# Optimization experiments

Measured on AMD Instinct MI355X. Metric: run time of the kernel, lower is better.

## Reference

```python
import jax, jax.numpy as jnp
import numpy as np

# ---- static config (mirrors Spectral2xDown.__init__) ----
B, C_IN, C_OUT = 2, 256, 256
H_HI, W_HI = 256, 512
H_LO, W_LO = 128, 256
LMAX = H_LO            # 128
MMAX = W_LO // 2 + 1   # 129
GROUPS = 32
EPS_GN = 1e-5


def _cc_nodes_weights(n):
    """Clenshaw-Curtis nodes x_j=cos(pi*j/(n-1)) and quadrature weights on [-1,1]
    (torch_harmonics 'equiangular' grid)."""
    N = n - 1
    tj = np.pi * np.arange(n) / N
    xj = np.cos(tj)
    ks = np.arange(1, N // 2 + 1)
    b = np.where(2 * ks == N, 1.0, 2.0)
    s = (b / (4.0 * ks**2 - 1.0))[None, :] * np.cos(2.0 * ks[None, :] * tj[:, None])
    w = (2.0 / N) * (1.0 - s.sum(axis=1))
    w[0] = w[-1] = (1.0 / N**2) if (N % 2) else (1.0 / (N**2 - 1.0))
    return xj, w


def _legpoly(mmax, lmax, x):
    """Orthonormal associated Legendre (-1)^m c_lm P_lm(x), shape [mmax,lmax,len(x)]
    (torch_harmonics _precompute_legpoly, norm='ortho', csphase=True)."""
    nmax = max(mmax, lmax)
    vdm = np.zeros((nmax, nmax, len(x)))
    vdm[0, 0] = 1.0 / np.sqrt(4.0 * np.pi)
    for l in range(1, nmax):
        vdm[l - 1, l] = np.sqrt(2 * l + 1) * x * vdm[l - 1, l - 1]
        vdm[l, l] = np.sqrt((2 * l + 1) * (1 + x) * (1 - x) / (2 * l)) * vdm[l - 1, l - 1]
    for l in range(2, nmax):
        for m in range(0, l - 1):
            vdm[m, l] = (x * np.sqrt((2 * l - 1) / (l - m) * (2 * l + 1) / (l + m)) * vdm[m, l - 1]
                         - np.sqrt((l + m - 1) / (l - m) * (2 * l + 1) / (2 * l - 3)
                                   * (l - m - 1) / (l + m)) * vdm[m, l - 2])
    vdm = vdm[:mmax, :lmax].copy()
    for m in range(1, mmax, 2):  # Condon-Shortley phase
        vdm[m] *= -1.0
    return vdm


def _precompute():
    ct_hi, w_hi = _cc_nodes_weights(H_HI)
    pct_hi = _legpoly(MMAX, LMAX, np.flip(np.arccos(ct_hi)) * 0 + np.cos(np.flip(np.arccos(ct_hi))))
    wmat_hi = pct_hi * w_hi[None, None, :]          # quadrature folded in: [M,L,K_hi]
    ct_lo, _ = _cc_nodes_weights(H_LO)
    pct_lo = _legpoly(MMAX, LMAX, np.cos(np.flip(np.arccos(ct_lo))))  # [M,L,K_lo]
    return wmat_hi.astype(np.float32), pct_lo.astype(np.float32)


def setup_inputs() -> dict:
    key = jax.random.key(0)
    k1, k2 = jax.random.split(key, 2)
    x = jax.random.normal(k1, (B, C_IN, H_HI, W_HI), jnp.float32)
    conv_w = jax.random.normal(k2, (C_OUT, C_IN), jnp.float32) / np.sqrt(C_IN)
    conv_b = jnp.zeros((C_OUT,), jnp.float32)
    gamma = jnp.ones((C_OUT,), jnp.float32)
    beta = jnp.zeros((C_OUT,), jnp.float32)
    wmat_hi, pct_lo = _precompute()
    return {"x": x, "conv_w": conv_w, "conv_b": conv_b, "gamma": gamma, "beta": beta,
            "wmat_hi": jnp.asarray(wmat_hi), "pct_lo": jnp.asarray(pct_lo)}


def reference(x, conv_w, conv_b, gamma, beta, wmat_hi, pct_lo):
    # --- forward real SHT on high-res grid (2*pi * rfft(norm='forward') + Legendre quadrature) ---
    X = (2.0 * jnp.pi / W_HI) * jnp.fft.rfft(x, axis=-1)     # [B,C,K_hi,W_HI//2+1]
    X = X[..., :MMAX]                                        # truncate to mmax
    flm_r = jnp.einsum('bckm,mlk->bclm', X.real, wmat_hi)    # [B,C,L,M]
    flm_i = jnp.einsum('bckm,mlk->bclm', X.imag, wmat_hi)
    # --- inverse real SHT on low-res grid ---
    g = (jnp.einsum('bclm,mlk->bckm', flm_r, pct_lo)
         + 1j * jnp.einsum('bclm,mlk->bckm', flm_i, pct_lo))  # [B,C,K_lo,M]
    y = jnp.fft.irfft(g, n=W_LO, axis=-1) * W_LO             # irfft norm='forward'
    # --- 1x1 conv -> GroupNorm(32) -> exact GELU ---
    h = jnp.einsum('bchw,oc->bohw', y, conv_w) + conv_b[None, :, None, None]
    hg = h.reshape(B, GROUPS, C_OUT // GROUPS, H_LO, W_LO)
    mu = hg.mean(axis=(2, 3, 4), keepdims=True)
    var = ((hg - mu) ** 2).mean(axis=(2, 3, 4), keepdims=True)
    hn = ((hg - mu) * jax.lax.rsqrt(var + EPS_GN)).reshape(B, C_OUT, H_LO, W_LO)
    out = hn * gamma[None, :, None, None] + beta[None, :, None, None]
    return jax.nn.gelu(out, approximate=False)
```

## Files before the change

### kernel.cpp

```cpp
#include <hip/hip_runtime.h>
#include <math.h>


#define ROWS_HI 131072
#define ROWS_LO 65536

#define B_FT    0LL
#define B_FIT   262144LL
#define B_WM    393216LL
#define B_PCT   8781824LL
#define B_WB    12976128LL
#define B_STATS 13107200LL
#define B_R1    13107712LL
#define B_R2    80216576LL

typedef __attribute__((ext_vector_type(8))) short bf16x8;
typedef __attribute__((ext_vector_type(8))) unsigned short ushort8;
typedef __attribute__((ext_vector_type(4))) unsigned short ushort4v;
typedef __attribute__((ext_vector_type(4))) float f32x4;

__device__ inline unsigned short f2bf(float f){
  unsigned int u = __float_as_uint(f);
  unsigned int r = u + 0x7FFFu + ((u >> 16) & 1u);
  return (unsigned short)(r >> 16);
}

__global__ __launch_bounds__(256) void k_tables(unsigned char* __restrict__ ws){
  unsigned short* FT  = (unsigned short*)(ws + B_FT);
  unsigned short* FIT = (unsigned short*)(ws + B_FIT);
  float* stats = (float*)(ws + B_STATS);
  int idx = blockIdx.x*256 + threadIdx.x;
  if (idx < 131072){
    int p = idx >> 9, w = idx & 511, m = p >> 1;
    int pr = (m*w) & 511;
    float ang = (float)pr * (float)(2.0*M_PI/512.0);
    float s, c; sincosf(ang, &s, &c);
    const float S = (float)(2.0*M_PI/512.0);
    FT[idx] = f2bf((p & 1) ? (-S*s) : (S*c));
  }
  int i2 = idx - 131072;
  if (i2 >= 0 && i2 < 65536){
    int w = i2 >> 8, p = i2 & 255, m = p >> 1;
    float eps = (m == 0) ? 1.f : 2.f;
    int pr = (m*w) & 255;
    float ang = (float)pr * (float)(2.0*M_PI/256.0);
    float s, c; sincosf(ang, &s, &c);
    FIT[i2] = f2bf((p & 1) ? (-eps*s) : (eps*c));
  }
  int i3 = idx - (131072 + 65536);
  if (i3 >= 0 && i3 < 128) stats[i3] = 0.f;
}

__global__ __launch_bounds__(256) void k_prep(const float* __restrict__ wmat,
                                              const float* __restrict__ pct,
                                              const float* __restrict__ Wc,
                                              unsigned char* __restrict__ ws){
  unsigned short* WM = (unsigned short*)(ws + B_WM);
  unsigned short* PT = (unsigned short*)(ws + B_PCT);
  unsigned short* WB = (unsigned short*)(ws + B_WB);
  int idx = blockIdx.x*256 + threadIdx.x;
  if (idx < 4194304){
    WM[idx] = f2bf(wmat[idx]);
  } else if (idx < 6291456){
    int j = idx - 4194304;
    int m = j >> 14, kp = (j >> 7) & 127, l = j & 127;
    PT[j] = f2bf(pct[m*16384 + l*128 + kp]);
  } else if (idx < 6356992){
    int j = idx - 6291456;
    WB[j] = f2bf(Wc[j]);
  }
}

template<int AMODE, int CMODE, bool BIAS, int MT, int NT, int SKIP>
__global__ __launch_bounds__(256) void k_gemm(
    const float* __restrict__ Af,
    const unsigned short* __restrict__ Abf,
    const unsigned short* __restrict__ Bt,
    float* __restrict__ Cf,
    unsigned short* __restrict__ Cbf,
    const float* __restrict__ bias,
    int ldA, int ldB, int ldC, int ksteps,
    long long sA, long long sB, int bzsh, long long sC)
{
  constexpr int BM = MT*32;
  constexpr int BN = NT*32;
  __shared__ unsigned short As[BM][40];
  __shared__ unsigned short Bs[BN][40];
  const int tid = threadIdx.x;
  const int z = blockIdx.z;
  const int m = z >> 1;
  const long long offA = (long long)z * sA;
  const long long offB = (long long)(z >> bzsh) * sB;
  const long long offC = (long long)z * sC;
  const int row0 = blockIdx.x * BM;
  const int n0   = blockIdx.y * BN;
  const int lane = tid & 63;
  const int wv = tid >> 6;
  const int wm = wv >> 1, wn = wv & 1;
  const int fr = lane & 15, q = lane >> 4;

  f32x4 acc[MT][NT];
#pragma unroll
  for (int i=0;i<MT;++i)
#pragma unroll
    for (int j=0;j<NT;++j) acc[i][j] = (f32x4){0.f,0.f,0.f,0.f};

  int ks0 = (SKIP == 2) ? (m >> 5) : 0;
  for (int ks = ks0; ks < ksteps; ++ks){
    const int k0 = ks * 32;
    if (AMODE == 0){
      const int row = tid >> 1, half = tid & 1;
      const float* s = Af + offA + (long long)(row0 + row) * ldA + k0 + half*16;
      float vv[16];
      *(float4*)(vv+0)  = *(const float4*)(s+0);
      *(float4*)(vv+4)  = *(const float4*)(s+4);
      *(float4*)(vv+8)  = *(const float4*)(s+8);
      *(float4*)(vv+12) = *(const float4*)(s+12);
      ushort8 H0, H1;
#pragma unroll
      for (int j=0;j<8;++j){ H0[j] = f2bf(vv[j]); H1[j] = f2bf(vv[8+j]); }
      *(ushort8*)&As[row][half*16]   = H0;
      *(ushort8*)&As[row][half*16+8] = H1;
    } else if (BM == 256){
      const unsigned short* s = Abf + offA + (long long)(row0 + tid) * ldA + k0;
      *(ushort8*)&As[tid][0]  = *(const ushort8*)(s);
      *(ushort8*)&As[tid][8]  = *(const ushort8*)(s+8);
      *(ushort8*)&As[tid][16] = *(const ushort8*)(s+16);
      *(ushort8*)&As[tid][24] = *(const ushort8*)(s+24);
    } else {
      const int row = tid >> 1, half = tid & 1;
      const unsigned short* s = Abf + offA + (long long)(row0 + row) * ldA + k0 + half*16;
      *(ushort8*)&As[row][half*16]   = *(const ushort8*)(s);
      *(ushort8*)&As[row][half*16+8] = *(const ushort8*)(s+8);
    }
    if (BN == 256){
      const unsigned short* s = Bt + offB + (long long)(n0 + tid) * ldB + k0;
      *(ushort8*)&Bs[tid][0]  = *(const ushort8*)(s);
      *(ushort8*)&Bs[tid][8]  = *(const ushort8*)(s+8);
      *(ushort8*)&Bs[tid][16] = *(const ushort8*)(s+16);
      *(ushort8*)&Bs[tid][24] = *(const ushort8*)(s+24);
    } else {
      const int row = tid >> 1, half = tid & 1;
      const unsigned short* s = Bt + offB + (long long)(n0 + row) * ldB + k0 + half*16;
      *(ushort8*)&Bs[row][half*16]   = *(const ushort8*)(s);
      *(ushort8*)&Bs[row][half*16+8] = *(const ushort8*)(s+8);
    }
    __syncthreads();
    bf16x8 ah[MT];
#pragma unroll
    for (int mt=0;mt<MT;++mt)
      ah[mt] = *(const bf16x8*)&As[wm*(MT*16)+mt*16+fr][q*8];
#pragma unroll
    for (int nt=0;nt<NT;++nt){
      if (SKIP == 1 && (wn*(NT*16) + nt*16 + 16 <= m)) continue;
      bf16x8 bb = *(const bf16x8*)&Bs[wn*(NT*16)+nt*16+fr][q*8];
#pragma unroll
      for (int mt=0;mt<MT;++mt)
        acc[mt][nt] = __builtin_amdgcn_mfma_f32_16x16x32_bf16(ah[mt], bb, acc[mt][nt], 0,0,0);
    }
    __syncthreads();
  }

  if (CMODE == 0){
#pragma unroll
    for (int mt=0;mt<MT;++mt){
      int row = row0 + wm*(MT*16) + mt*16 + q*4;
      float bv0=0.f,bv1=0.f,bv2=0.f,bv3=0.f;
      if (BIAS){ bv0=bias[row]; bv1=bias[row+1]; bv2=bias[row+2]; bv3=bias[row+3]; }
#pragma unroll
      for (int nt=0;nt<NT;++nt){
        int col = n0 + wn*(NT*16) + nt*16 + fr;
        float* dst = Cf + offC + (long long)row * ldC + col;
        dst[0]                = acc[mt][nt][0] + bv0;
        dst[(long long)ldC]   = acc[mt][nt][1] + bv1;
        dst[(long long)ldC*2] = acc[mt][nt][2] + bv2;
        dst[(long long)ldC*3] = acc[mt][nt][3] + bv3;
      }
    }
  } else if (CMODE == 1){
#pragma unroll
    for (int nt=0;nt<NT;++nt){
      int colp = n0 + wn*(NT*16) + nt*16 + fr;
#pragma unroll
      for (int mt=0;mt<MT;++mt){
        int rowb = row0 + wm*(MT*16) + mt*16 + q*4;
        ushort4v h;
        h[0] = f2bf(acc[mt][nt][0]);
        h[1] = f2bf(acc[mt][nt][1]);
        h[2] = f2bf(acc[mt][nt][2]);
        h[3] = f2bf(acc[mt][nt][3]);
        *(ushort4v*)&Cbf[offC + (long long)colp * ldC + rowb] = h;
      }
    }
  } else {
#pragma unroll
    for (int mt=0;mt<MT;++mt){
      int row = row0 + wm*(MT*16) + mt*16 + q*4;
#pragma unroll
      for (int nt=0;nt<NT;++nt){
        int col = n0 + wn*(NT*16) + nt*16 + fr;
        unsigned short* dst = Cbf + offC + (long long)row * ldC + col;
        dst[0]      = f2bf(acc[mt][nt][0]);
        dst[ldC]    = f2bf(acc[mt][nt][1]);
        dst[ldC*2]  = f2bf(acc[mt][nt][2]);
        dst[ldC*3]  = f2bf(acc[mt][nt][3]);
      }
    }
  }
}

__global__ __launch_bounds__(256) void k_trb(const unsigned short* __restrict__ g,
                                             unsigned short* __restrict__ gT){
  __shared__ unsigned short t[64][68];
  const int r0 = blockIdx.x * 64;
  const int p0 = blockIdx.y * 64;
  const int tr = threadIdx.x & 15, tc = threadIdx.x >> 4;
#pragma unroll
  for (int i=0;i<4;++i){
    int pl = tc + i*16;
    ushort4v v = *(const ushort4v*)(g + (long long)(p0+pl)*ROWS_LO + r0 + tr*4);
    *(ushort4v*)&t[pl][tr*4] = v;
  }
  __syncthreads();
#pragma unroll
  for (int i=0;i<4;++i){
    int rl = tc + i*16;
    ushort4v w;
    w[0]=t[tr*4+0][rl]; w[1]=t[tr*4+1][rl]; w[2]=t[tr*4+2][rl]; w[3]=t[tr*4+3][rl];
    *(ushort4v*)(gT + (long long)(r0+rl)*256 + p0 + tr*4) = w;
  }
}

__global__ __launch_bounds__(256) void k_tr2(const float* __restrict__ y,
                                             unsigned short* __restrict__ yT){
  __shared__ float t[64][65];
  const int s0 = blockIdx.x * 64;
  const int c0 = blockIdx.y * 64;
  const int b  = blockIdx.z;
  const int tr = threadIdx.x & 15, tc = threadIdx.x >> 4;
#pragma unroll
  for (int i=0;i<4;++i){
    int cl = tc + i*16;
    float4 v = *(const float4*)(y + (long long)b*8388608 + (long long)(c0+cl)*32768 + s0 + tr*4);
    t[cl][tr*4+0]=v.x; t[cl][tr*4+1]=v.y; t[cl][tr*4+2]=v.z; t[cl][tr*4+3]=v.w;
  }
  __syncthreads();
#pragma unroll
  for (int i=0;i<4;++i){
    int sl = tc + i*16;
    ushort4v w;
    w[0]=f2bf(t[tr*4+0][sl]); w[1]=f2bf(t[tr*4+1][sl]);
    w[2]=f2bf(t[tr*4+2][sl]); w[3]=f2bf(t[tr*4+3][sl]);
    *(ushort4v*)(yT + (long long)b*8388608 + (long long)(s0+sl)*256 + c0 + tr*4) = w;
  }
}

__global__ __launch_bounds__(256) void k_stats(const float* __restrict__ h,
                                               float* __restrict__ stats){
  const int bg = blockIdx.y;
  const int j  = blockIdx.x;
  const int t  = threadIdx.x;
  const float* base = h + (long long)bg*262144 + j*8192;
  float s = 0.f, ss = 0.f;
#pragma unroll
  for (int i=0;i<8;++i){
    float4 v = *(const float4*)(base + i*1024 + t*4);
    s  += v.x + v.y + v.z + v.w;
    ss += v.x*v.x + v.y*v.y + v.z*v.z + v.w*v.w;
  }
#pragma unroll
  for (int off=32; off>0; off>>=1){
    s  += __shfl_down(s, off, 64);
    ss += __shfl_down(ss, off, 64);
  }
  __shared__ float red[8];
  int wid = t >> 6;
  if ((t & 63) == 0){ red[wid*2] = s; red[wid*2+1] = ss; }
  __syncthreads();
  if (t == 0){
    float S  = red[0]+red[2]+red[4]+red[6];
    float SS = red[1]+red[3]+red[5]+red[7];
    atomicAdd(&stats[bg*2+0], S);
    atomicAdd(&stats[bg*2+1], SS);
  }
}

__global__ __launch_bounds__(256) void k_norm(float* __restrict__ out,
                                              const float* __restrict__ stats,
                                              const float* __restrict__ gamma,
                                              const float* __restrict__ beta){
  long long idx4 = ((long long)blockIdx.x*256 + threadIdx.x)*4;
  int o = (int)((idx4 >> 15) & 255);
  int b = (int)(idx4 >> 23);
  int bg = b*32 + (o >> 3);
  const float inv_n = 1.0f/262144.0f;
  float mean = stats[bg*2+0] * inv_n;
  float var  = stats[bg*2+1] * inv_n - mean*mean;
  float sc = rsqrtf(var + 1e-5f);
  float ga = gamma[o], be = beta[o];
  float4 v = *(float4*)(out + idx4);
  float t0 = (v.x - mean)*sc*ga + be;
  float t1 = (v.y - mean)*sc*ga + be;
  float t2 = (v.z - mean)*sc*ga + be;
  float t3 = (v.w - mean)*sc*ga + be;
  const float ISQ2 = 0.70710678118654752f;
  v.x = 0.5f*t0*(1.0f + erff(t0*ISQ2));
  v.y = 0.5f*t1*(1.0f + erff(t1*ISQ2));
  v.z = 0.5f*t2*(1.0f + erff(t2*ISQ2));
  v.w = 0.5f*t3*(1.0f + erff(t3*ISQ2));
  *(float4*)(out + idx4) = v;
}

extern "C" void kernel_launch(void* const* d_in, const int* in_sizes, int n_in,
                              void* d_out, int out_size, void* d_ws, size_t ws_size,
                              hipStream_t stream){
  const float* x      = (const float*)d_in[0];
  const float* conv_w = (const float*)d_in[1];
  const float* conv_b = (const float*)d_in[2];
  const float* gamma  = (const float*)d_in[3];
  const float* beta   = (const float*)d_in[4];
  const float* wmat   = (const float*)d_in[5];
  const float* pct    = (const float*)d_in[6];
  unsigned char* ws = (unsigned char*)d_ws;

  unsigned short* FT   = (unsigned short*)(ws + B_FT);
  unsigned short* FIT  = (unsigned short*)(ws + B_FIT);
  unsigned short* WM   = (unsigned short*)(ws + B_WM);
  unsigned short* PT   = (unsigned short*)(ws + B_PCT);
  unsigned short* WB   = (unsigned short*)(ws + B_WB);
  float*          stats= (float*)(ws + B_STATS);
  unsigned short* Xbf  = (unsigned short*)(ws + B_R1);
  unsigned short* gb   = (unsigned short*)(ws + B_R1);
  float*          y    = (float*)(ws + B_R1);
  unsigned short* flmb = (unsigned short*)(ws + B_R2);
  unsigned short* gTb  = (unsigned short*)(ws + B_R2);
  unsigned short* yT   = (unsigned short*)(ws + B_R2);
  float* out = (float*)d_out;

  k_tables<<<769, 256, 0, stream>>>(ws);
  k_prep  <<<24832, 256, 0, stream>>>(wmat, pct, conv_w, ws);

  k_gemm<0,1,false,4,8,0><<<dim3(1024,1,1), 256, 0, stream>>>(
      x, nullptr, FT, nullptr, Xbf, nullptr, 512, 512, ROWS_HI, 16, 0, 0, 0, 0);
  k_gemm<1,2,false,4,4,1><<<dim3(4,1,256), 256, 0, stream>>>(
      nullptr, Xbf, WM, nullptr, flmb, nullptr, 256, 256, 128, 8,
      131072LL, 32768LL, 1, 65536LL);
  k_gemm<1,2,false,4,4,2><<<dim3(4,1,256), 256, 0, stream>>>(
      nullptr, flmb, PT, nullptr, gb, nullptr, 128, 128, 128, 4,
      65536LL, 16384LL, 1, 65536LL);
  k_trb<<<dim3(1024,4), 256, 0, stream>>>(gb, gTb);
  k_gemm<1,0,false,4,8,0><<<dim3(512,1,1), 256, 0, stream>>>(
      nullptr, gTb, FIT, y, nullptr, nullptr, 256, 256, 256, 8, 0, 0, 0, 0);
  k_tr2<<<dim3(512,4,2), 256, 0, stream>>>(y, yT);
  k_gemm<1,0,true,8,4,0><<<dim3(1,256,2), 256, 0, stream>>>(
      nullptr, WB, yT, out, nullptr, conv_b, 256, 256, 32768, 8,
      0, 8388608LL, 0, 8388608LL);

  k_stats<<<dim3(32,64), 256, 0, stream>>>(out, stats);
  k_norm <<<16384, 256, 0, stream>>>(out, stats, gamma, beta);
}
```

Measured before the change: 672.7 us.

## Fold forward and inverse Legendre matrices into one precomputed operator; use direct LDS loads

Multiplies the per-m inverse Legendre table by the forward quadrature matrix once per call, so the two chained per-m GEMMs become a single 256-to-128 GEMM on the Fourier coefficients. GEMM staging now uses global_load_lds 16-byte async copies into unpadded LDS tiles, with a fixed 128x128 tile and an occupancy hint. Workspace buffers stop aliasing each other. The fused operator is built in bf16, which adds rounding to the combined matrix, drops the triangular skip optimizations, and the unpadded LDS rows may cause bank conflicts.

```diff
diff --git a/kernel.cpp b/kernel.cpp
--- a/kernel.cpp
+++ b/kernel.cpp
@@ -11,8 +11,13 @@
 #define B_PCT   8781824LL
 #define B_WB    12976128LL
 #define B_STATS 13107200LL
-#define B_R1    13107712LL
-#define B_R2    80216576LL
+#define B_WMT   13107712LL
+#define B_QM    21496320LL
+#define B_XBF   29884928LL
+#define B_GB    96993792LL
+#define B_GTB   130548224LL
+#define B_Y     164102656LL
+#define B_YT    231211520LL
 
 typedef __attribute__((ext_vector_type(8))) short bf16x8;
 typedef __attribute__((ext_vector_type(8))) unsigned short ushort8;
@@ -23,6 +28,12 @@
   unsigned int u = __float_as_uint(f);
   unsigned int r = u + 0x7FFFu + ((u >> 16) & 1u);
   return (unsigned short)(r >> 16);
+}
+
+__device__ inline void gl_lds16(const unsigned short* g, unsigned short* l){
+  __builtin_amdgcn_global_load_lds(
+      (const __attribute__((address_space(1))) unsigned int*)g,
+      (__attribute__((address_space(3))) unsigned int*)l, 16, 0, 0);
 }
 
 __global__ __launch_bounds__(256) void k_tables(unsigned char* __restrict__ ws){
@@ -55,9 +66,10 @@
                                               const float* __restrict__ pct,
                                               const float* __restrict__ Wc,
                                               unsigned char* __restrict__ ws){
-  unsigned short* WM = (unsigned short*)(ws + B_WM);
-  unsigned short* PT = (unsigned short*)(ws + B_PCT);
-  unsigned short* WB = (unsigned short*)(ws + B_WB);
+  unsigned short* WM  = (unsigned short*)(ws + B_WM);
+  unsigned short* PT  = (unsigned short*)(ws + B_PCT);
+  unsigned short* WB  = (unsigned short*)(ws + B_WB);
+  unsigned short* WMT = (unsigned short*)(ws + B_WMT);
   int idx = blockIdx.x*256 + threadIdx.x;
   if (idx < 4194304){
     WM[idx] = f2bf(wmat[idx]);
@@ -68,11 +80,15 @@
   } else if (idx < 6356992){
     int j = idx - 6291456;
     WB[j] = f2bf(Wc[j]);
-  }
-}
-
-template<int AMODE, int CMODE, bool BIAS, int MT, int NT, int SKIP>
-__global__ __launch_bounds__(256) void k_gemm(
+  } else if (idx < 10551296){
+    int j = idx - 6356992;
+    int m = j >> 15, k = (j >> 7) & 255, l = j & 127;
+    WMT[j] = f2bf(wmat[m*32768 + l*256 + k]);
+  }
+}
+
+template<int AMODE, int CMODE, bool BIAS, int SKIP, int MZSH, int WPE>
+__global__ __launch_bounds__(256, WPE) void k_gemm(
     const float* __restrict__ Af,
     const unsigned short* __restrict__ Abf,
     const unsigned short* __restrict__ Bt,
@@ -82,30 +98,29 @@
     int ldA, int ldB, int ldC, int ksteps,
     long long sA, long long sB, int bzsh, long long sC)
 {
-  constexpr int BM = MT*32;
-  constexpr int BN = NT*32;
-  __shared__ unsigned short As[BM][40];
-  __shared__ unsigned short Bs[BN][40];
+  __shared__ __align__(16) unsigned short As[128][32];
+  __shared__ __align__(16) unsigned short Bs[128][32];
   const int tid = threadIdx.x;
   const int z = blockIdx.z;
-  const int m = z >> 1;
+  const int m = z >> MZSH;
   const long long offA = (long long)z * sA;
   const long long offB = (long long)(z >> bzsh) * sB;
   const long long offC = (long long)z * sC;
-  const int row0 = blockIdx.x * BM;
-  const int n0   = blockIdx.y * BN;
+  const int row0 = blockIdx.x * 128;
+  const int n0   = blockIdx.y * 128;
   const int lane = tid & 63;
   const int wv = tid >> 6;
   const int wm = wv >> 1, wn = wv & 1;
   const int fr = lane & 15, q = lane >> 4;
-
-  f32x4 acc[MT][NT];
-#pragma unroll
-  for (int i=0;i<MT;++i)
-#pragma unroll
-    for (int j=0;j<NT;++j) acc[i][j] = (f32x4){0.f,0.f,0.f,0.f};
-
-  int ks0 = (SKIP == 2) ? (m >> 5) : 0;
+  const int srow = tid >> 2, skb = tid & 3;
+
+  f32x4 acc[4][4];
+#pragma unroll
+  for (int i=0;i<4;++i)
+#pragma unroll
+    for (int j=0;j<4;++j) acc[i][j] = (f32x4){0.f,0.f,0.f,0.f};
+
+  const int ks0 = (SKIP == 2) ? (m >> 5) : 0;
   for (int ks = ks0; ks < ksteps; ++ks){
     const int k0 = ks * 32;
     if (AMODE == 0){
@@ -121,41 +136,28 @@
       for (int j=0;j<8;++j){ H0[j] = f2bf(vv[j]); H1[j] = f2bf(vv[8+j]); }
       *(ushort8*)&As[row][half*16]   = H0;
       *(ushort8*)&As[row][half*16+8] = H1;
-    } else if (BM == 256){
-      const unsigned short* s = Abf + offA + (long long)(row0 + tid) * ldA + k0;
-      *(ushort8*)&As[tid][0]  = *(const ushort8*)(s);
-      *(ushort8*)&As[tid][8]  = *(const ushort8*)(s+8);
-      *(ushort8*)&As[tid][16] = *(const ushort8*)(s+16);
-      *(ushort8*)&As[tid][24] = *(const ushort8*)(s+24);
     } else {
-      const int row = tid >> 1, half = tid & 1;
-      const unsigned short* s = Abf + offA + (long long)(row0 + row) * ldA + k0 + half*16;
-      *(ushort8*)&As[row][half*16]   = *(const ushort8*)(s);
-      *(ushort8*)&As[row][half*16+8] = *(const ushort8*)(s+8);
-    }
-    if (BN == 256){
-      const unsigned short* s = Bt + offB + (long long)(n0 + tid) * ldB + k0;
-      *(ushort8*)&Bs[tid][0]  = *(const ushort8*)(s);
-      *(ushort8*)&Bs[tid][8]  = *(const ushort8*)(s+8);
-      *(ushort8*)&Bs[tid][16] = *(const ushort8*)(s+16);
-      *(ushort8*)&Bs[tid][24] = *(const ushort8*)(s+24);
-    } else {
-      const int row = tid >> 1, half = tid & 1;
-      const unsigned short* s = Bt + offB + (long long)(n0 + row) * ldB + k0 + half*16;
-      *(ushort8*)&Bs[row][half*16]   = *(const ushort8*)(s);
-      *(ushort8*)&Bs[row][half*16+8] = *(const ushort8*)(s+8);
+#pragma unroll
+      for (int i=0;i<2;++i){
+        const unsigned short* g = Abf + offA + (long long)(row0 + i*64 + srow) * ldA + k0 + skb*8;
+        gl_lds16(g, (unsigned short*)As + i*2048 + wv*512);
+      }
+    }
+#pragma unroll
+    for (int i=0;i<2;++i){
+      const unsigned short* g = Bt + offB + (long long)(n0 + i*64 + srow) * ldB + k0 + skb*8;
+      gl_lds16(g, (unsigned short*)Bs + i*2048 + wv*512);
     }
     __syncthreads();
-    bf16x8 ah[MT];
-#pragma unroll
-    for (int mt=0;mt<MT;++mt)
-      ah[mt] = *(const bf16x8*)&As[wm*(MT*16)+mt*16+fr][q*8];
-#pragma unroll
-    for (int nt=0;nt<NT;++nt){
-      if (SKIP == 1 && (wn*(NT*16) + nt*16 + 16 <= m)) continue;
-      bf16x8 bb = *(const bf16x8*)&Bs[wn*(NT*16)+nt*16+fr][q*8];
-#pragma unroll
-      for (int mt=0;mt<MT;++mt)
+    bf16x8 ah[4];
+#pragma unroll
+    for (int mt=0;mt<4;++mt)
+      ah[mt] = *(const bf16x8*)&As[wm*64 + mt*16 + fr][q*8];
+#pragma unroll
+    for (int nt=0;nt<4;++nt){
+      bf16x8 bb = *(const bf16x8*)&Bs[wn*64 + nt*16 + fr][q*8];
+#pragma unroll
+      for (int mt=0;mt<4;++mt)
         acc[mt][nt] = __builtin_amdgcn_mfma_f32_16x16x32_bf16(ah[mt], bb, acc[mt][nt], 0,0,0);
     }
     __syncthreads();
@@ -163,13 +165,13 @@
 
   if (CMODE == 0){
 #pragma unroll
-    for (int mt=0;mt<MT;++mt){
-      int row = row0 + wm*(MT*16) + mt*16 + q*4;
+    for (int mt=0;mt<4;++mt){
+      int row = row0 + wm*64 + mt*16 + q*4;
       float bv0=0.f,bv1=0.f,bv2=0.f,bv3=0.f;
       if (BIAS){ bv0=bias[row]; bv1=bias[row+1]; bv2=bias[row+2]; bv3=bias[row+3]; }
 #pragma unroll
-      for (int nt=0;nt<NT;++nt){
-        int col = n0 + wn*(NT*16) + nt*16 + fr;
+      for (int nt=0;nt<4;++nt){
+        int col = n0 + wn*64 + nt*16 + fr;
         float* dst = Cf + offC + (long long)row * ldC + col;
         dst[0]                = acc[mt][nt][0] + bv0;
         dst[(long long)ldC]   = acc[mt][nt][1] + bv1;
@@ -179,11 +181,11 @@
     }
   } else if (CMODE == 1){
 #pragma unroll
-    for (int nt=0;nt<NT;++nt){
-      int colp = n0 + wn*(NT*16) + nt*16 + fr;
-#pragma unroll
-      for (int mt=0;mt<MT;++mt){
-        int rowb = row0 + wm*(MT*16) + mt*16 + q*4;
+    for (int nt=0;nt<4;++nt){
+      int colp = n0 + wn*64 + nt*16 + fr;
+#pragma unroll
+      for (int mt=0;mt<4;++mt){
+        int rowb = row0 + wm*64 + mt*16 + q*4;
         ushort4v h;
         h[0] = f2bf(acc[mt][nt][0]);
         h[1] = f2bf(acc[mt][nt][1]);
@@ -194,11 +196,11 @@
     }
   } else {
 #pragma unroll
-    for (int mt=0;mt<MT;++mt){
-      int row = row0 + wm*(MT*16) + mt*16 + q*4;
-#pragma unroll
-      for (int nt=0;nt<NT;++nt){
-        int col = n0 + wn*(NT*16) + nt*16 + fr;
+    for (int mt=0;mt<4;++mt){
+      int row = row0 + wm*64 + mt*16 + q*4;
+#pragma unroll
+      for (int nt=0;nt<4;++nt){
+        int col = n0 + wn*64 + nt*16 + fr;
         unsigned short* dst = Cbf + offC + (long long)row * ldC + col;
         dst[0]      = f2bf(acc[mt][nt][0]);
         dst[ldC]    = f2bf(acc[mt][nt][1]);
@@ -325,34 +327,40 @@
 
   unsigned short* FT   = (unsigned short*)(ws + B_FT);
   unsigned short* FIT  = (unsigned short*)(ws + B_FIT);
-  unsigned short* WM   = (unsigned short*)(ws + B_WM);
   unsigned short* PT   = (unsigned short*)(ws + B_PCT);
   unsigned short* WB   = (unsigned short*)(ws + B_WB);
+  unsigned short* WMT  = (unsigned short*)(ws + B_WMT);
+  unsigned short* QM   = (unsigned short*)(ws + B_QM);
   float*          stats= (float*)(ws + B_STATS);
-  unsigned short* Xbf  = (unsigned short*)(ws + B_R1);
-  unsigned short* gb   = (unsigned short*)(ws + B_R1);
-  float*          y    = (float*)(ws + B_R1);
-  unsigned short* flmb = (unsigned short*)(ws + B_R2);
-  unsigned short* gTb  = (unsigned short*)(ws + B_R2);
-  unsigned short* yT   = (unsigned short*)(ws + B_R2);
+  unsigned short* Xbf  = (unsigned short*)(ws + B_XBF);
+  unsigned short* gb   = (unsigned short*)(ws + B_GB);
+  unsigned short* gTb  = (unsigned short*)(ws + B_GTB);
+  float*          y    = (float*)(ws + B_Y);
+  unsigned short* yT   = (unsigned short*)(ws + B_YT);
   float* out = (float*)d_out;
 
   k_tables<<<769, 256, 0, stream>>>(ws);
-  k_prep  <<<24832, 256, 0, stream>>>(wmat, pct, conv_w, ws);
-
-  k_gemm<0,1,false,4,8,0><<<dim3(1024,1,1), 256, 0, stream>>>(
+  k_prep  <<<41216, 256, 0, stream>>>(wmat, pct, conv_w, ws);
+
+  k_gemm<1,2,false,2,0,3><<<dim3(1,2,128), 256, 0, stream>>>(
+      nullptr, PT, WMT, nullptr, QM, nullptr, 128, 128, 256, 4,
+      16384LL, 32768LL, 0, 32768LL);
+
+  k_gemm<0,1,false,0,0,3><<<dim3(1024,2,1), 256, 0, stream>>>(
       x, nullptr, FT, nullptr, Xbf, nullptr, 512, 512, ROWS_HI, 16, 0, 0, 0, 0);
-  k_gemm<1,2,false,4,4,1><<<dim3(4,1,256), 256, 0, stream>>>(
-      nullptr, Xbf, WM, nullptr, flmb, nullptr, 256, 256, 128, 8,
+
+  k_gemm<1,2,false,0,0,3><<<dim3(4,1,256), 256, 0, stream>>>(
+      nullptr, Xbf, QM, nullptr, gb, nullptr, 256, 256, 128, 8,
       131072LL, 32768LL, 1, 65536LL);
-  k_gemm<1,2,false,4,4,2><<<dim3(4,1,256), 256, 0, stream>>>(
-      nullptr, flmb, PT, nullptr, gb, nullptr, 128, 128, 128, 4,
-      65536LL, 16384LL, 1, 65536LL);
+
   k_trb<<<dim3(1024,4), 256, 0, stream>>>(gb, gTb);
-  k_gemm<1,0,false,4,8,0><<<dim3(512,1,1), 256, 0, stream>>>(
+
+  k_gemm<1,0,false,0,0,3><<<dim3(512,2,1), 256, 0, stream>>>(
       nullptr, gTb, FIT, y, nullptr, nullptr, 256, 256, 256, 8, 0, 0, 0, 0);
+
   k_tr2<<<dim3(512,4,2), 256, 0, stream>>>(y, yT);
-  k_gemm<1,0,true,8,4,0><<<dim3(1,256,2), 256, 0, stream>>>(
+
+  k_gemm<1,0,true,0,0,3><<<dim3(2,256,2), 256, 0, stream>>>(
       nullptr, WB, yT, out, nullptr, conv_b, 256, 256, 32768, 8,
       0, 8388608LL, 0, 8388608LL);
 
```

After: 653.3 us. 1.03x faster.
